# Kernel tuning notes

Measured on AMD Instinct MI355X. Metric: run time of the kernel, lower is better.

Reference implementation:

```python
import jax, jax.numpy as jnp
import numpy as np

T, B, NHID = 64, 32, 768
NB, BS = 6, 128          # num_blocks, block_size = nhid // num_blocks
TOPK = 4                 # active blocks per step
NTOK = 32000
ATT = 4 * BS             # input-attention value dim (att_out), per RIMs BlocksCore
DK = 64                  # input-attention key dim
NH2, DK2 = 4, 16         # communication attention heads / head dim


def setup_inputs() -> dict:
    key = jax.random.key(0)
    ks = jax.random.split(key, 16)
    s = 0.02
    return {
        "x": jax.random.normal(ks[0], (T, B, NHID), jnp.float32),
        "hx0": jax.random.normal(ks[1], (B, NHID), jnp.float32),
        "cx0": jax.random.normal(ks[2], (B, NHID), jnp.float32),
        # input attention (1 head): per-read-block query proj, per-write-slot key/value proj
        "Wq_in": jax.random.normal(ks[3], (NB, BS, DK), jnp.float32) * s,
        "Wk_in": jax.random.normal(ks[4], (2, NHID, DK), jnp.float32) * s,
        "Wv_in": jax.random.normal(ks[5], (2, NHID, ATT), jnp.float32) * s,
        # block-diagonal LSTM (blockify_params): per-block weights
        "Wih": jax.random.normal(ks[6], (NB, ATT, 4 * BS), jnp.float32) * s,
        "Whh": jax.random.normal(ks[7], (NB, BS, 4 * BS), jnp.float32) * s,
        "b_lstm": jnp.zeros((NB, 4 * BS), jnp.float32),
        # communication attention (4 heads, dk=dv=16), per-block projections + output proj
        "Wq_c": jax.random.normal(ks[8], (NB, BS, NH2 * DK2), jnp.float32) * s,
        "Wk_c": jax.random.normal(ks[9], (NB, BS, NH2 * DK2), jnp.float32) * s,
        "Wv_c": jax.random.normal(ks[10], (NB, BS, NH2 * DK2), jnp.float32) * s,
        "Wo_c": jax.random.normal(ks[11], (NB, NH2 * DK2, BS), jnp.float32) * s,
        # decoder
        "Wd": jax.random.normal(ks[12], (NTOK, NHID), jnp.float32) * 0.1,
        "bd": jnp.zeros((NTOK,), jnp.float32),
    }


def _step(hx, cx, xt, Wq_in, Wk_in, Wv_in, Wih, Whh, b_lstm, Wq_c, Wk_c, Wv_c, Wo_c):
    hb = hx.reshape(B, NB, BS)
    cb = cx.reshape(B, NB, BS)
    # --- input attention: each block reads from {null, input} slots ---
    kv_in = jnp.stack([jnp.zeros_like(xt), xt], axis=1)          # [B,2,NHID]
    q = jnp.einsum('bnd,ndk->bnk', hb, Wq_in)                    # [B,NB,DK]
    k = jnp.einsum('bmd,mdk->bmk', kv_in, Wk_in)                 # [B,2,DK]
    v = jnp.einsum('bmd,mdv->bmv', kv_in, Wv_in)                 # [B,2,ATT]
    iatt = jax.nn.softmax(
        jnp.einsum('bnk,bmk->bnm', q, k) / jnp.sqrt(jnp.float32(DK)), axis=-1)
    inp_use = jnp.einsum('bnm,bmv->bnv', iatt, v)                # [B,NB,ATT]
    # --- top-k block routing: drop NB-TOPK blocks attending most to null ---
    null_att = iatt[:, :, 0]                                     # [B,NB]
    _, drop_idx = jax.lax.top_k(null_att, NB - TOPK)
    mask = jnp.ones((B, NB), hx.dtype).at[
        jnp.arange(B)[:, None], drop_idx].set(0.0)               # [B,NB]
    # --- per-block (block-diagonal) LSTM ---
    gates = (jnp.einsum('bnv,nvg->bng', inp_use, Wih)
             + jnp.einsum('bnh,nhg->bng', hb, Whh) + b_lstm)     # [B,NB,4*BS]
    i, f, g, o = jnp.split(gates, 4, axis=-1)
    c_new = jax.nn.sigmoid(f) * cb + jax.nn.sigmoid(i) * jnp.tanh(g)
    h_new = jax.nn.sigmoid(o) * jnp.tanh(c_new)                  # [B,NB,BS]
    # --- communication attention among blocks (residual) ---
    q2 = jnp.einsum('bnd,ndk->bnk', h_new, Wq_c).reshape(B, NB, NH2, DK2)
    k2 = jnp.einsum('bnd,ndk->bnk', h_new, Wk_c).reshape(B, NB, NH2, DK2)
    v2 = jnp.einsum('bnd,ndk->bnk', h_new, Wv_c).reshape(B, NB, NH2, DK2)
    att = jax.nn.softmax(
        jnp.einsum('bihk,bjhk->bhij', q2, k2) / jnp.sqrt(jnp.float32(DK2)), axis=-1)
    comm = jnp.einsum('bhij,bjhv->bihv', att, v2).reshape(B, NB, NH2 * DK2)
    h_new = h_new + jnp.einsum('bnk,nkd->bnd', comm, Wo_c)
    # --- gated state update: inactive blocks keep old state ---
    m = mask[:, :, None]
    hx_next = (m * h_new + (1.0 - m) * hb).reshape(B, NHID)
    cx_next = (m * c_new + (1.0 - m) * cb).reshape(B, NHID)
    return hx_next, cx_next


def reference(x, hx0, cx0, Wq_in, Wk_in, Wv_in, Wih, Whh, b_lstm,
              Wq_c, Wk_c, Wv_c, Wo_c, Wd, bd):
    def scan_step(carry, xt):
        hx, cx = carry
        hx, cx = _step(hx, cx, xt, Wq_in, Wk_in, Wv_in, Wih, Whh, b_lstm,
                       Wq_c, Wk_c, Wv_c, Wo_c)
        return (hx, cx), hx
    (hx, cx), outs = jax.lax.scan(scan_step, (hx0, cx0), x)     # outs: [T,B,NHID]
    decoded = outs.reshape(T * B, NHID) @ Wd.T + bd              # [T*B,NTOK]
    return decoded, hx, cx
```

## Files before the change

kernel.cpp:

```cpp
#include <hip/hip_runtime.h>
#include <hip/hip_bf16.h>
#include <stdint.h>

#define TT 64
#define BB 32
#define NHIDC 768
#define NBK 6
#define BSZ 128
#define NTOKC 32000

using f32x4  = __attribute__((ext_vector_type(4))) float;
using f32x2  = __attribute__((ext_vector_type(2))) float;
using short8 = __attribute__((ext_vector_type(8))) short;
typedef unsigned long long u64;

#define OFF_XPUB  4096u
#define OFF_HTB   8065024u
#define OFF_K1    11210752u
#define OFF_V1    11735040u
#define OFF_U     15929344u
#define OFF_WDB   41095168u

__device__ __forceinline__ float sigf(float x){ return 1.f/(1.f + expf(-x)); }

__device__ __forceinline__ void stp(u64* p, float v, unsigned tag){
  union { float f; unsigned u; } cv; cv.f = v;
  const u64 pk = ((u64)tag << 32) | cv.u;
  __hip_atomic_store(p, pk, __ATOMIC_RELAXED, __HIP_MEMORY_SCOPE_AGENT);
}
__device__ __forceinline__ float ldp(const u64* p, unsigned tag){
  u64 v = __hip_atomic_load(p, __ATOMIC_RELAXED, __HIP_MEMORY_SCOPE_AGENT);
  while ((unsigned)(v >> 32) < tag){
    __builtin_amdgcn_s_sleep(1);
    v = __hip_atomic_load(p, __ATOMIC_RELAXED, __HIP_MEMORY_SCOPE_AGENT);
  }
  union { unsigned u; float f; } cv; cv.u = (unsigned)v;
  return cv.f;
}
#define CBAR asm volatile("" ::: "memory")

__device__ __forceinline__ void gload16(const void* g, void* l){
  __builtin_amdgcn_global_load_lds(
      (const __attribute__((address_space(1))) unsigned int*)g,
      (__attribute__((address_space(3))) unsigned int*)l, 16, 0, 0);
}

__device__ __forceinline__ int xslot(int par, int gg, int nn, int b){
  return (((par*16 + gg)*6 + nn)*2 + b)*132;
}

__global__ void prep_kernel(const float* __restrict__ Wd,
                            unsigned short* __restrict__ Wdb,
                            u64* __restrict__ xpub)
{
  {
    int i = blockIdx.x*blockDim.x + threadIdx.x;
    const int nx = 2*16*6*2*132;
    const int stride = gridDim.x*blockDim.x;
    for (; i < nx; i += stride)
      __hip_atomic_store(xpub + i, 0ull, __ATOMIC_RELAXED, __HIP_MEMORY_SCOPE_AGENT);
  }
  int i = blockIdx.x*blockDim.x + threadIdx.x;
  const int n4 = NTOKC*NHIDC/4;
  const int stride = gridDim.x*blockDim.x;
  for (; i < n4; i += stride){
    const float4 v = ((const float4*)Wd)[i];
    ushort4 o;
    __hip_bfloat16 b0 = __float2bfloat16(v.x); o.x = *reinterpret_cast<unsigned short*>(&b0);
    __hip_bfloat16 b1 = __float2bfloat16(v.y); o.y = *reinterpret_cast<unsigned short*>(&b1);
    __hip_bfloat16 b2 = __float2bfloat16(v.z); o.z = *reinterpret_cast<unsigned short*>(&b2);
    __hip_bfloat16 b3 = __float2bfloat16(v.w); o.w = *reinterpret_cast<unsigned short*>(&b3);
    ((ushort4*)Wdb)[i] = o;
  }
}

template<int TM, int TN>
__global__ __launch_bounds__(256) void gemm_f32(
    const float* __restrict__ A, int lda,
    const float* __restrict__ B, int ldb, long bstride,
    float* __restrict__ C, int ldc, long cstride,
    int N, int K)
{
  constexpr int BM = 16*TM, BN = 16*TN;
  __shared__ float As[16][BM];
  __shared__ float Bs[16][BN+4];
  const float* Bb = B + (long)blockIdx.z * bstride;
  float* Cb = C + (long)blockIdx.z * cstride;
  const int m0 = blockIdx.x*BM, n0 = blockIdx.y*BN;
  const int tid = threadIdx.x, tx = tid & 15, ty = tid >> 4;
  float acc[TM][TN];
  #pragma unroll
  for (int i=0;i<TM;++i)
    #pragma unroll
    for (int j=0;j<TN;++j) acc[i][j]=0.f;

  for (int k0=0; k0<K; k0+=16){
    if constexpr (TM == 8){
      const int r = tid>>1, kk = (tid&1)*8;
      const float4 v0 = *(const float4*)&A[(long)(m0+r)*lda + k0 + kk];
      const float4 v1 = *(const float4*)&A[(long)(m0+r)*lda + k0 + kk + 4];
      As[kk+0][r]=v0.x; As[kk+1][r]=v0.y; As[kk+2][r]=v0.z; As[kk+3][r]=v0.w;
      As[kk+4][r]=v1.x; As[kk+5][r]=v1.y; As[kk+6][r]=v1.z; As[kk+7][r]=v1.w;
    } else {
      const int r = tid>>2, kk = (tid&3)*4;
      const float4 v0 = *(const float4*)&A[(long)(m0+r)*lda + k0 + kk];
      As[kk+0][r]=v0.x; As[kk+1][r]=v0.y; As[kk+2][r]=v0.z; As[kk+3][r]=v0.w;
    }
    if constexpr (TN == 8){
      const int rb = tid>>4, cb = (tid&15)*8;
      float4 v0 = {0,0,0,0}, v1 = {0,0,0,0};
      if (n0+cb+4 <= N) v0 = *(const float4*)&Bb[(long)(k0+rb)*ldb + n0+cb];
      if (n0+cb+8 <= N) v1 = *(const float4*)&Bb[(long)(k0+rb)*ldb + n0+cb+4];
      *(float4*)&Bs[rb][cb]   = v0;
      *(float4*)&Bs[rb][cb+4] = v1;
    } else {
      const int rb = tid>>4, cb = (tid&15)*4;
      float4 v0 = {0,0,0,0};
      if (n0+cb+4 <= N) v0 = *(const float4*)&Bb[(long)(k0+rb)*ldb + n0+cb];
      *(float4*)&Bs[rb][cb] = v0;
    }
    __syncthreads();
    #pragma unroll
    for (int kk=0; kk<16; ++kk){
      float av[TM], bv[TN];
      #pragma unroll
      for (int i=0;i<TM;++i) av[i] = As[kk][ty*TM+i];
      #pragma unroll
      for (int j=0;j<TN;++j) bv[j] = Bs[kk][tx*TN+j];
      #pragma unroll
      for (int i=0;i<TM;++i)
        #pragma unroll
        for (int j=0;j<TN;++j) acc[i][j] += av[i]*bv[j];
    }
    __syncthreads();
  }
  #pragma unroll
  for (int i=0;i<TM;++i){
    const int row = m0 + ty*TM + i;
    #pragma unroll
    for (int j=0;j<TN;++j){
      const int col = n0 + tx*TN + j;
      if (col < N) Cb[(long)row*ldc + col] = acc[i][j];
    }
  }
}

__global__ __launch_bounds__(1024, 2) void recurrent_kernel(
    const float* __restrict__ hx0, const float* __restrict__ cx0,
    const float* __restrict__ Wq_in, const float* __restrict__ Whh,
    const float* __restrict__ b_lstm,
    const float* __restrict__ Wk_c, const float* __restrict__ Wv_c,
    const float* __restrict__ Wq_c, const float* __restrict__ Wo_c,
    const float* __restrict__ K1buf, const float* __restrict__ Ubuf,
    u64* __restrict__ xpub,
    unsigned short* __restrict__ HTx,
    float* __restrict__ out_hx, float* __restrict__ out_cx)
{
  const int w = blockIdx.x, gg = w/6, n = w - gg*6, tid = threadIdx.x;

  __shared__ float WcT[192*130];
  __shared__ float WqL[128*65];
  __shared__ float hL[2][128], cL[2][128], h0L[2][128], cnL[2][128];
  __shared__ float partL[2][2][512];
  __shared__ float uL[2][512];
  __shared__ float blL[512];
  __shared__ float kvqL[2][192];
  __shared__ float kvAll[2][6][130];
  __shared__ float commL[2][64];
  __shared__ float nullAll[2][8];
  __shared__ float sL[2], nullLoc[2], maskL[2];

  const int kh = tid >> 9, gc = tid & 511;
  const int od = tid >> 3, okq = tid & 7;

  f32x4 whr[16];
  {
    const float* src = Whh + (long)n*65536 + kh*64*512 + gc;
    #pragma unroll
    for (int r4=0; r4<16; ++r4){
      f32x4 v;
      v[0] = src[(r4*4+0)*512]; v[1] = src[(r4*4+1)*512];
      v[2] = src[(r4*4+2)*512]; v[3] = src[(r4*4+3)*512];
      whr[r4] = v;
    }
  }
  #pragma unroll
  for (int i=0;i<16;++i) asm volatile("" : "+v"(whr[i]));
  f32x4 wo0, wo1;
  {
    const float* src = Wo_c + n*8192 + od;
    #pragma unroll
    for (int j=0;j<4;++j) wo0[j] = src[(okq*8+j)*128];
    #pragma unroll
    for (int j=0;j<4;++j) wo1[j] = src[(okq*8+4+j)*128];
  }
  asm volatile("" : "+v"(wo0));
  asm volatile("" : "+v"(wo1));

  if (tid < 512) blL[tid] = b_lstm[n*512 + tid];
  for (int i = tid; i < 8192; i += 1024){
    const int h = i>>6, c = i&63;
    WcT[(c    )*130 + h] = Wk_c[n*8192 + i];
    WcT[(c+ 64)*130 + h] = Wv_c[n*8192 + i];
    WcT[(c+128)*130 + h] = Wq_c[n*8192 + i];
    WqL[h*65 + c] = Wq_in[n*8192 + i];
  }
  if (tid < 256){
    const int b = tid>>7, d = tid&127;
    hL[b][d] = hx0[(gg*2+b)*768 + n*128 + d];
    cL[b][d] = cx0[(gg*2+b)*768 + n*128 + d];
  }
  __syncthreads();

  for (int t = 0; t < TT; ++t){
    const int par = t & 1;
    const unsigned tag = (unsigned)(t+1);
    uL[kh][gc] = Ubuf[((long)(t*32 + gg*2 + kh)*6 + n)*512 + gc];
    float k1r = 0.f;
    if (tid < 128) k1r = K1buf[(long)(t*32 + gg*2 + (tid>>6))*64 + (tid&63)];

    {
      float gd0 = 0.f, gd1 = 0.f;
      #pragma unroll
      for (int r4 = 0; r4 < 16; ++r4){
        const f32x4 h0v = *(const f32x4*)&hL[0][kh*64 + r4*4];
        const f32x4 h1v = *(const f32x4*)&hL[1][kh*64 + r4*4];
        #pragma unroll
        for (int j=0;j<4;++j){
          gd0 += whr[r4][j]*h0v[j];
          gd1 += whr[r4][j]*h1v[j];
        }
      }
      partL[0][kh][gc] = gd0;
      partL[1][kh][gc] = gd1;
    }
    if (tid < 128){
      const int b = tid>>6, k = tid&63;
      float q = 0.f;
      #pragma unroll 16
      for (int h=0; h<128; ++h) q += WqL[h*65 + k]*hL[b][h];
      float term = q*k1r;
      #pragma unroll
      for (int off=32; off; off>>=1) term += __shfl_xor(term, off);
      if (k == 0){
        const float l1 = term*0.125f;
        const float mx = fmaxf(l1, 0.f);
        const float e0 = expf(0.f-mx), e1 = expf(l1-mx);
        const float inv = 1.f/(e0+e1);
        sL[b] = e1*inv;
        nullLoc[b] = e0*inv;
        stp(xpub + xslot(par,gg,n,b) + 128, e0*inv, tag);
      }
    }
    __syncthreads();
    if (tid < 256){
      const int b = tid>>7, dd = tid&127;
      const float s = sL[b];
      const float gi = partL[b][0][dd]     + partL[b][1][dd]     + s*uL[b][dd]     + blL[dd];
      const float gf = partL[b][0][128+dd] + partL[b][1][128+dd] + s*uL[b][128+dd] + blL[128+dd];
      const float gG = partL[b][0][256+dd] + partL[b][1][256+dd] + s*uL[b][256+dd] + blL[256+dd];
      const float go = partL[b][0][384+dd] + partL[b][1][384+dd] + s*uL[b][384+dd] + blL[384+dd];
      const float cp = cL[b][dd];
      const float cn = sigf(gf)*cp + sigf(gi)*tanhf(gG);
      const float h0 = sigf(go)*tanhf(cn);
      cnL[b][dd] = cn; h0L[b][dd] = h0;
    }
    __syncthreads();
    if (tid < 384){
      const int b = tid/192, c = tid%192;
      float a = 0.f;
      #pragma unroll
      for (int h4=0; h4<32; ++h4){
        const f32x2 wa = *(const f32x2*)&WcT[c*130 + h4*4];
        const f32x2 wb = *(const f32x2*)&WcT[c*130 + h4*4 + 2];
        const f32x4 hv = *(const f32x4*)&h0L[b][h4*4];
        a += wa[0]*hv[0] + wa[1]*hv[1] + wb[0]*hv[2] + wb[1]*hv[3];
      }
      kvqL[b][c] = a;
      if (c < 128) stp(xpub + xslot(par,gg,n,b) + c, a, tag);
    }
    __syncthreads();
    for (int idx = tid; idx < 1536; idx += 1024){
      const int j = idx/256, r = idx&255, b = r>>7, c = r&127;
      if (j == n) kvAll[b][j][c] = kvqL[b][c];
      else        kvAll[b][j][c] = ldp(xpub + xslot(par,gg,j,b) + c, tag);
    }
    if (tid < 12){
      const int j = tid>>1, b = tid&1;
      if (j == n) nullAll[b][j] = nullLoc[b];
      else        nullAll[b][j] = ldp(xpub + xslot(par,gg,j,b) + 128, tag);
    }
    __syncthreads(); CBAR;
    if (tid < 64){
      const int lane = tid;
      const int g5 = lane>>3, l3 = lane&7;
      const int b = g5>>2, h = g5&3;
      float lg = -1e30f;
      if (l3 < 6){
        float s = 0.f;
        #pragma unroll
        for (int kk=0; kk<16; ++kk)
          s += kvqL[b][128 + h*16 + kk]*kvAll[b][l3][h*16 + kk];
        lg = s*0.25f;
      }
      float mx = lg;
      mx = fmaxf(mx, __shfl_xor(mx,1));
      mx = fmaxf(mx, __shfl_xor(mx,2));
      mx = fmaxf(mx, __shfl_xor(mx,4));
      float ev = (l3 < 6) ? expf(lg - mx) : 0.f;
      float sum = ev;
      sum += __shfl_xor(sum,1); sum += __shfl_xor(sum,2); sum += __shfl_xor(sum,4);
      const float myw = ev/sum;
      float s0 = 0.f, s1 = 0.f;
      #pragma unroll
      for (int j=0;j<6;++j){
        const float wj = __shfl(myw, g5*8 + j);
        s0 += wj*kvAll[b][j][64 + h*16 + l3*2];
        s1 += wj*kvAll[b][j][64 + h*16 + l3*2 + 1];
      }
      commL[b][h*16 + l3*2]     = s0;
      commL[b][h*16 + l3*2 + 1] = s1;
      if (lane < 2){
        const float own = nullAll[lane][n];
        int rank = 0;
        #pragma unroll
        for (int j=0;j<6;++j){
          const float v = nullAll[lane][j];
          rank += (v > own || (v == own && j < n)) ? 1 : 0;
        }
        maskL[lane] = (rank < 2) ? 0.f : 1.f;
      }
    }
    __syncthreads();
    {
      #pragma unroll
      for (int b=0; b<2; ++b){
        float a = 0.f;
        #pragma unroll
        for (int j=0;j<4;++j) a += commL[b][okq*8+j]*wo0[j];
        #pragma unroll
        for (int j=0;j<4;++j) a += commL[b][okq*8+4+j]*wo1[j];
        a += __shfl_xor(a,1); a += __shfl_xor(a,2); a += __shfl_xor(a,4);
        if (okq == 0 && maskL[b] != 0.f){
          hL[b][od] = h0L[b][od] + a;
          cL[b][od] = cnL[b][od];
        }
      }
    }
    __syncthreads();
    if (tid < 256){
      const int b = tid>>7, d = tid&127;
      const float hv = hL[b][d];
      __hip_bfloat16 hb16 = __float2bfloat16(hv);
      HTx[(long)(t*32 + gg*2 + b)*768 + n*128 + d] = *reinterpret_cast<unsigned short*>(&hb16);
      if (t == TT-1){
        out_hx[(gg*2+b)*768 + n*128 + d] = hv;
        out_cx[(gg*2+b)*768 + n*128 + d] = cL[b][d];
      }
    }
  }
}

__global__ __launch_bounds__(256) void decoder_kernel(
    const unsigned short* __restrict__ A,
    const unsigned short* __restrict__ Bw,
    const float* __restrict__ bd,
    float* __restrict__ out)
{
  __shared__ unsigned short As[4096];
  __shared__ unsigned short Bs[4096];
  const int bid = blockIdx.x;
  const int tile = (bid & 7)*500 + (bid >> 3);
  const int m0 = (tile & 15)*128, n0 = (tile >> 4)*128;
  const int tid = threadIdx.x;
  const int wv = tid >> 6, lane = tid & 63;
  const int wm = wv >> 1, wn = wv & 1;
  const int r16 = lane & 15, krow = lane >> 4;

  f32x4 acc[4][4] = {};

  for (int k0 = 0; k0 < 768; k0 += 32){
    #pragma unroll
    for (int i=0; i<2; ++i){
      const int idx = i*256 + tid;
      const int row = idx >> 2, k8 = (idx & 3)*8;
      gload16(&A [(long)(m0+row)*768 + k0 + k8], (char*)As + i*4096 + wv*1024);
      gload16(&Bw[(long)(n0+row)*768 + k0 + k8], (char*)Bs + i*4096 + wv*1024);
    }
    __syncthreads();
    short8 af[4], bf[4];
    #pragma unroll
    for (int mi=0; mi<4; ++mi)
      af[mi] = *(const short8*)&As[(wm*64 + mi*16 + r16)*32 + krow*8];
    #pragma unroll
    for (int ni=0; ni<4; ++ni)
      bf[ni] = *(const short8*)&Bs[(wn*64 + ni*16 + r16)*32 + krow*8];
    #pragma unroll
    for (int mi=0; mi<4; ++mi)
      #pragma unroll
      for (int ni=0; ni<4; ++ni)
        acc[mi][ni] = __builtin_amdgcn_mfma_f32_16x16x32_bf16(af[mi], bf[ni], acc[mi][ni], 0, 0, 0);
    __syncthreads();
  }

  #pragma unroll
  for (int ni=0; ni<4; ++ni){
    const int col = n0 + wn*64 + ni*16 + r16;
    const float bv = bd[col];
    #pragma unroll
    for (int mi=0; mi<4; ++mi){
      const int rbase = m0 + wm*64 + mi*16 + krow*4;
      #pragma unroll
      for (int j=0; j<4; ++j)
        out[(size_t)(rbase + j)*NTOKC + col] = acc[mi][ni][j] + bv;
    }
  }
}

extern "C" void kernel_launch(void* const* d_in, const int* in_sizes, int n_in,
                              void* d_out, int out_size, void* d_ws, size_t ws_size,
                              hipStream_t stream)
{
  (void)in_sizes; (void)n_in; (void)out_size; (void)ws_size;
  const float* x      = (const float*)d_in[0];
  const float* hx0    = (const float*)d_in[1];
  const float* cx0    = (const float*)d_in[2];
  const float* Wq_in  = (const float*)d_in[3];
  const float* Wk_in  = (const float*)d_in[4];
  const float* Wv_in  = (const float*)d_in[5];
  const float* Wih    = (const float*)d_in[6];
  const float* Whh    = (const float*)d_in[7];
  const float* b_lstm = (const float*)d_in[8];
  const float* Wq_c   = (const float*)d_in[9];
  const float* Wk_c   = (const float*)d_in[10];
  const float* Wv_c   = (const float*)d_in[11];
  const float* Wo_c   = (const float*)d_in[12];
  const float* Wd     = (const float*)d_in[13];
  const float* bd     = (const float*)d_in[14];

  char* ws = (char*)d_ws;
  u64*           xpub = (u64*)(ws + OFF_XPUB);
  unsigned short* HTx = (unsigned short*)(ws + OFF_HTB);
  float*         K1b  = (float*)(ws + OFF_K1);
  float*         V1b  = (float*)(ws + OFF_V1);
  float*         Ub   = (float*)(ws + OFF_U);
  unsigned short* Wdb = (unsigned short*)(ws + OFF_WDB);

  float* out_dec = (float*)d_out;
  float* out_hx  = out_dec + (size_t)2048*NTOKC;
  float* out_cx  = out_hx + BB*NHIDC;

  prep_kernel<<<2048, 256, 0, stream>>>(Wd, Wdb, xpub);
  gemm_f32<4,4><<<dim3(32,1,1), 256, 0, stream>>>(x, NHIDC, Wk_in + 768*64, 64, 0,
                                                  K1b, 64, 0, 64, NHIDC);
  gemm_f32<4,4><<<dim3(32,8,1), 256, 0, stream>>>(x, NHIDC, Wv_in + 768*512, 512, 0,
                                                  V1b, 512, 0, 512, NHIDC);
  gemm_f32<8,8><<<dim3(16,4,6), 256, 0, stream>>>(V1b, 512, Wih, 512, (long)512*512,
                                                  Ub, 3072, 512, 512, 512);
  recurrent_kernel<<<96, 1024, 0, stream>>>(hx0, cx0, Wq_in, Whh, b_lstm,
                                            Wk_c, Wv_c, Wq_c, Wo_c,
                                            K1b, Ub, xpub, HTx,
                                            out_hx, out_cx);
  decoder_kernel<<<4000, 256, 0, stream>>>(HTx, Wdb, bd, out_dec);
}
```

Measured before the change: 1.273 ms.

## Fuse all stages into a persistent mega-kernel overlapping recurrence with decoder

Replaces the separate prep, projection GEMMs, recurrent and decoder launches with one persistent kernel. 96 blocks run the recurrence while 160 worker blocks convert Wd to bf16, compute the input projections, and then pull decoder tiles dynamically. Each decoder tile waits on per-4-step counters, so the decoder for finished timesteps overlaps the remaining recurrence. The intent is to hide the decoder and prep work behind the serial recurrence and remove launch gaps. The cost is spin-wait synchronisation through global atomics and a co-residency assumption for all 256 blocks, which can deadlock if they are not all resident.

```diff
diff --git a/kernel.cpp b/kernel.cpp
--- a/kernel.cpp
+++ b/kernel.cpp
@@ -8,12 +8,16 @@
 #define NBK 6
 #define BSZ 128
 #define NTOKC 32000
+#define NREC 96
+#define NWRK 160
+#define NWG  256
 
 using f32x4  = __attribute__((ext_vector_type(4))) float;
 using f32x2  = __attribute__((ext_vector_type(2))) float;
 using short8 = __attribute__((ext_vector_type(8))) short;
 typedef unsigned long long u64;
 
+#define OFF_CTR   0u
 #define OFF_XPUB  4096u
 #define OFF_HTB   8065024u
 #define OFF_K1    11210752u
@@ -37,6 +41,13 @@
   union { unsigned u; float f; } cv; cv.u = (unsigned)v;
   return cv.f;
 }
+__device__ __forceinline__ void stc(float* p, float v){
+  __hip_atomic_store(p, v, __ATOMIC_RELAXED, __HIP_MEMORY_SCOPE_AGENT);
+}
+__device__ __forceinline__ void waitc(unsigned int* p, unsigned tgt){
+  while (__hip_atomic_load(p, __ATOMIC_RELAXED, __HIP_MEMORY_SCOPE_AGENT) < tgt)
+    __builtin_amdgcn_s_sleep(2);
+}
 #define CBAR asm volatile("" ::: "memory")
 
 __device__ __forceinline__ void gload16(const void* g, void* l){
@@ -49,45 +60,50 @@
   return (((par*16 + gg)*6 + nn)*2 + b)*132;
 }
 
-__global__ void prep_kernel(const float* __restrict__ Wd,
-                            unsigned short* __restrict__ Wdb,
-                            u64* __restrict__ xpub)
-{
-  {
-    int i = blockIdx.x*blockDim.x + threadIdx.x;
-    const int nx = 2*16*6*2*132;
-    const int stride = gridDim.x*blockDim.x;
-    for (; i < nx; i += stride)
-      __hip_atomic_store(xpub + i, 0ull, __ATOMIC_RELAXED, __HIP_MEMORY_SCOPE_AGENT);
-  }
+struct RecS {
+  float WcT[192*130];
+  float WqL[128*65];
+  float hL[2][128], cL[2][128], h0L[2][128], cnL[2][128];
+  float partL[2][2][512];
+  float uL[2][512];
+  float blL[512];
+  float kvqL[2][192];
+  float kvAll[2][6][130];
+  float commL[2][64];
+  float nullAll[2][8];
+  float sL[2], nullLoc[2], maskL[2];
+};
+struct WrkS {
+  union {
+    struct { float As[4][16][128]; float Bs[4][16][132]; } g8;
+    struct { float As[4][16][64];  float Bs[4][16][68];  } g4;
+    struct { unsigned short As[4][4096]; unsigned short Bs[4][4096]; } d;
+  };
+  int bcast;
+};
+union SmemU { RecS r; WrkS w; };
+
+__global__ void prep0_kernel(unsigned int* __restrict__ ctr, u64* __restrict__ xpub){
   int i = blockIdx.x*blockDim.x + threadIdx.x;
-  const int n4 = NTOKC*NHIDC/4;
+  if (i < 64)
+    __hip_atomic_store(&ctr[i], 0u, __ATOMIC_RELAXED, __HIP_MEMORY_SCOPE_AGENT);
+  const int nx = 2*16*6*2*132;
   const int stride = gridDim.x*blockDim.x;
-  for (; i < n4; i += stride){
-    const float4 v = ((const float4*)Wd)[i];
-    ushort4 o;
-    __hip_bfloat16 b0 = __float2bfloat16(v.x); o.x = *reinterpret_cast<unsigned short*>(&b0);
-    __hip_bfloat16 b1 = __float2bfloat16(v.y); o.y = *reinterpret_cast<unsigned short*>(&b1);
-    __hip_bfloat16 b2 = __float2bfloat16(v.z); o.z = *reinterpret_cast<unsigned short*>(&b2);
-    __hip_bfloat16 b3 = __float2bfloat16(v.w); o.w = *reinterpret_cast<unsigned short*>(&b3);
-    ((ushort4*)Wdb)[i] = o;
-  }
+  for (int j = i; j < nx; j += stride)
+    __hip_atomic_store(&xpub[j], 0ull, __ATOMIC_RELAXED, __HIP_MEMORY_SCOPE_AGENT);
 }
 
 template<int TM, int TN>
-__global__ __launch_bounds__(256) void gemm_f32(
-    const float* __restrict__ A, int lda,
-    const float* __restrict__ B, int ldb, long bstride,
-    float* __restrict__ C, int ldc, long cstride,
-    int N, int K)
+__device__ void gemm_unit(const float* __restrict__ A, int lda,
+                          const float* __restrict__ Bb, int ldb,
+                          float* __restrict__ Cb, int ldc,
+                          int N, int K, int m0, int n0, bool active,
+                          float* AsP, float* BsP, int ltid)
 {
   constexpr int BM = 16*TM, BN = 16*TN;
-  __shared__ float As[16][BM];
-  __shared__ float Bs[16][BN+4];
-  const float* Bb = B + (long)blockIdx.z * bstride;
-  float* Cb = C + (long)blockIdx.z * cstride;
-  const int m0 = blockIdx.x*BM, n0 = blockIdx.y*BN;
-  const int tid = threadIdx.x, tx = tid & 15, ty = tid >> 4;
+  float (*As)[BM]   = reinterpret_cast<float(*)[BM]>(AsP);
+  float (*Bs)[BN+4] = reinterpret_cast<float(*)[BN+4]>(BsP);
+  const int tx = ltid & 15, ty = ltid >> 4;
   float acc[TM][TN];
   #pragma unroll
   for (int i=0;i<TM;++i)
@@ -96,25 +112,25 @@
 
   for (int k0=0; k0<K; k0+=16){
     if constexpr (TM == 8){
-      const int r = tid>>1, kk = (tid&1)*8;
+      const int r = ltid>>1, kk = (ltid&1)*8;
       const float4 v0 = *(const float4*)&A[(long)(m0+r)*lda + k0 + kk];
       const float4 v1 = *(const float4*)&A[(long)(m0+r)*lda + k0 + kk + 4];
       As[kk+0][r]=v0.x; As[kk+1][r]=v0.y; As[kk+2][r]=v0.z; As[kk+3][r]=v0.w;
       As[kk+4][r]=v1.x; As[kk+5][r]=v1.y; As[kk+6][r]=v1.z; As[kk+7][r]=v1.w;
     } else {
-      const int r = tid>>2, kk = (tid&3)*4;
+      const int r = ltid>>2, kk = (ltid&3)*4;
       const float4 v0 = *(const float4*)&A[(long)(m0+r)*lda + k0 + kk];
       As[kk+0][r]=v0.x; As[kk+1][r]=v0.y; As[kk+2][r]=v0.z; As[kk+3][r]=v0.w;
     }
     if constexpr (TN == 8){
-      const int rb = tid>>4, cb = (tid&15)*8;
+      const int rb = ltid>>4, cb = (ltid&15)*8;
       float4 v0 = {0,0,0,0}, v1 = {0,0,0,0};
       if (n0+cb+4 <= N) v0 = *(const float4*)&Bb[(long)(k0+rb)*ldb + n0+cb];
       if (n0+cb+8 <= N) v1 = *(const float4*)&Bb[(long)(k0+rb)*ldb + n0+cb+4];
       *(float4*)&Bs[rb][cb]   = v0;
       *(float4*)&Bs[rb][cb+4] = v1;
     } else {
-      const int rb = tid>>4, cb = (tid&15)*4;
+      const int rb = ltid>>4, cb = (ltid&15)*4;
       float4 v0 = {0,0,0,0};
       if (n0+cb+4 <= N) v0 = *(const float4*)&Bb[(long)(k0+rb)*ldb + n0+cb];
       *(float4*)&Bs[rb][cb] = v0;
@@ -134,267 +150,47 @@
     }
     __syncthreads();
   }
-  #pragma unroll
-  for (int i=0;i<TM;++i){
-    const int row = m0 + ty*TM + i;
-    #pragma unroll
-    for (int j=0;j<TN;++j){
-      const int col = n0 + tx*TN + j;
-      if (col < N) Cb[(long)row*ldc + col] = acc[i][j];
+  if (active){
+    #pragma unroll
+    for (int i=0;i<TM;++i){
+      const int row = m0 + ty*TM + i;
+      #pragma unroll
+      for (int j=0;j<TN;++j){
+        const int col = n0 + tx*TN + j;
+        if (col < N) stc(&Cb[(long)row*ldc + col], acc[i][j]);
+      }
     }
   }
 }
 
-__global__ __launch_bounds__(1024, 2) void recurrent_kernel(
-    const float* __restrict__ hx0, const float* __restrict__ cx0,
-    const float* __restrict__ Wq_in, const float* __restrict__ Whh,
-    const float* __restrict__ b_lstm,
-    const float* __restrict__ Wk_c, const float* __restrict__ Wv_c,
-    const float* __restrict__ Wq_c, const float* __restrict__ Wo_c,
-    const float* __restrict__ K1buf, const float* __restrict__ Ubuf,
-    u64* __restrict__ xpub,
-    unsigned short* __restrict__ HTx,
-    float* __restrict__ out_hx, float* __restrict__ out_cx)
+__device__ void decoder_unit(const unsigned short* __restrict__ A,
+                             const unsigned short* __restrict__ Bw,
+                             const float* __restrict__ bd,
+                             float* __restrict__ out,
+                             int m0, int n0,
+                             unsigned short* AsP, unsigned short* BsP, int ltid)
 {
-  const int w = blockIdx.x, gg = w/6, n = w - gg*6, tid = threadIdx.x;
-
-  __shared__ float WcT[192*130];
-  __shared__ float WqL[128*65];
-  __shared__ float hL[2][128], cL[2][128], h0L[2][128], cnL[2][128];
-  __shared__ float partL[2][2][512];
-  __shared__ float uL[2][512];
-  __shared__ float blL[512];
-  __shared__ float kvqL[2][192];
-  __shared__ float kvAll[2][6][130];
-  __shared__ float commL[2][64];
-  __shared__ float nullAll[2][8];
-  __shared__ float sL[2], nullLoc[2], maskL[2];
-
-  const int kh = tid >> 9, gc = tid & 511;
-  const int od = tid >> 3, okq = tid & 7;
-
-  f32x4 whr[16];
-  {
-    const float* src = Whh + (long)n*65536 + kh*64*512 + gc;
-    #pragma unroll
-    for (int r4=0; r4<16; ++r4){
-      f32x4 v;
-      v[0] = src[(r4*4+0)*512]; v[1] = src[(r4*4+1)*512];
-      v[2] = src[(r4*4+2)*512]; v[3] = src[(r4*4+3)*512];
-      whr[r4] = v;
-    }
-  }
-  #pragma unroll
-  for (int i=0;i<16;++i) asm volatile("" : "+v"(whr[i]));
-  f32x4 wo0, wo1;
-  {
-    const float* src = Wo_c + n*8192 + od;
-    #pragma unroll
-    for (int j=0;j<4;++j) wo0[j] = src[(okq*8+j)*128];
-    #pragma unroll
-    for (int j=0;j<4;++j) wo1[j] = src[(okq*8+4+j)*128];
-  }
-  asm volatile("" : "+v"(wo0));
-  asm volatile("" : "+v"(wo1));
-
-  if (tid < 512) blL[tid] = b_lstm[n*512 + tid];
-  for (int i = tid; i < 8192; i += 1024){
-    const int h = i>>6, c = i&63;
-    WcT[(c    )*130 + h] = Wk_c[n*8192 + i];
-    WcT[(c+ 64)*130 + h] = Wv_c[n*8192 + i];
-    WcT[(c+128)*130 + h] = Wq_c[n*8192 + i];
-    WqL[h*65 + c] = Wq_in[n*8192 + i];
-  }
-  if (tid < 256){
-    const int b = tid>>7, d = tid&127;
-    hL[b][d] = hx0[(gg*2+b)*768 + n*128 + d];
-    cL[b][d] = cx0[(gg*2+b)*768 + n*128 + d];
-  }
-  __syncthreads();
-
-  for (int t = 0; t < TT; ++t){
-    const int par = t & 1;
-    const unsigned tag = (unsigned)(t+1);
-    uL[kh][gc] = Ubuf[((long)(t*32 + gg*2 + kh)*6 + n)*512 + gc];
-    float k1r = 0.f;
-    if (tid < 128) k1r = K1buf[(long)(t*32 + gg*2 + (tid>>6))*64 + (tid&63)];
-
-    {
-      float gd0 = 0.f, gd1 = 0.f;
-      #pragma unroll
-      for (int r4 = 0; r4 < 16; ++r4){
-        const f32x4 h0v = *(const f32x4*)&hL[0][kh*64 + r4*4];
-        const f32x4 h1v = *(const f32x4*)&hL[1][kh*64 + r4*4];
-        #pragma unroll
-        for (int j=0;j<4;++j){
-          gd0 += whr[r4][j]*h0v[j];
-          gd1 += whr[r4][j]*h1v[j];
-        }
-      }
-      partL[0][kh][gc] = gd0;
-      partL[1][kh][gc] = gd1;
-    }
-    if (tid < 128){
-      const int b = tid>>6, k = tid&63;
-      float q = 0.f;
-      #pragma unroll 16
-      for (int h=0; h<128; ++h) q += WqL[h*65 + k]*hL[b][h];
-      float term = q*k1r;
-      #pragma unroll
-      for (int off=32; off; off>>=1) term += __shfl_xor(term, off);
-      if (k == 0){
-        const float l1 = term*0.125f;
-        const float mx = fmaxf(l1, 0.f);
-        const float e0 = expf(0.f-mx), e1 = expf(l1-mx);
-        const float inv = 1.f/(e0+e1);
-        sL[b] = e1*inv;
-        nullLoc[b] = e0*inv;
-        stp(xpub + xslot(par,gg,n,b) + 128, e0*inv, tag);
-      }
-    }
-    __syncthreads();
-    if (tid < 256){
-      const int b = tid>>7, dd = tid&127;
-      const float s = sL[b];
-      const float gi = partL[b][0][dd]     + partL[b][1][dd]     + s*uL[b][dd]     + blL[dd];
-      const float gf = partL[b][0][128+dd] + partL[b][1][128+dd] + s*uL[b][128+dd] + blL[128+dd];
-      const float gG = partL[b][0][256+dd] + partL[b][1][256+dd] + s*uL[b][256+dd] + blL[256+dd];
-      const float go = partL[b][0][384+dd] + partL[b][1][384+dd] + s*uL[b][384+dd] + blL[384+dd];
-      const float cp = cL[b][dd];
-      const float cn = sigf(gf)*cp + sigf(gi)*tanhf(gG);
-      const float h0 = sigf(go)*tanhf(cn);
-      cnL[b][dd] = cn; h0L[b][dd] = h0;
-    }
-    __syncthreads();
-    if (tid < 384){
-      const int b = tid/192, c = tid%192;
-      float a = 0.f;
-      #pragma unroll
-      for (int h4=0; h4<32; ++h4){
-        const f32x2 wa = *(const f32x2*)&WcT[c*130 + h4*4];
-        const f32x2 wb = *(const f32x2*)&WcT[c*130 + h4*4 + 2];
-        const f32x4 hv = *(const f32x4*)&h0L[b][h4*4];
-        a += wa[0]*hv[0] + wa[1]*hv[1] + wb[0]*hv[2] + wb[1]*hv[3];
-      }
-      kvqL[b][c] = a;
-      if (c < 128) stp(xpub + xslot(par,gg,n,b) + c, a, tag);
-    }
-    __syncthreads();
-    for (int idx = tid; idx < 1536; idx += 1024){
-      const int j = idx/256, r = idx&255, b = r>>7, c = r&127;
-      if (j == n) kvAll[b][j][c] = kvqL[b][c];
-      else        kvAll[b][j][c] = ldp(xpub + xslot(par,gg,j,b) + c, tag);
-    }
-    if (tid < 12){
-      const int j = tid>>1, b = tid&1;
-      if (j == n) nullAll[b][j] = nullLoc[b];
-      else        nullAll[b][j] = ldp(xpub + xslot(par,gg,j,b) + 128, tag);
-    }
-    __syncthreads(); CBAR;
-    if (tid < 64){
-      const int lane = tid;
-      const int g5 = lane>>3, l3 = lane&7;
-      const int b = g5>>2, h = g5&3;
-      float lg = -1e30f;
-      if (l3 < 6){
-        float s = 0.f;
-        #pragma unroll
-        for (int kk=0; kk<16; ++kk)
-          s += kvqL[b][128 + h*16 + kk]*kvAll[b][l3][h*16 + kk];
-        lg = s*0.25f;
-      }
-      float mx = lg;
-      mx = fmaxf(mx, __shfl_xor(mx,1));
-      mx = fmaxf(mx, __shfl_xor(mx,2));
-      mx = fmaxf(mx, __shfl_xor(mx,4));
-      float ev = (l3 < 6) ? expf(lg - mx) : 0.f;
-      float sum = ev;
-      sum += __shfl_xor(sum,1); sum += __shfl_xor(sum,2); sum += __shfl_xor(sum,4);
-      const float myw = ev/sum;
-      float s0 = 0.f, s1 = 0.f;
-      #pragma unroll
-      for (int j=0;j<6;++j){
-        const float wj = __shfl(myw, g5*8 + j);
-        s0 += wj*kvAll[b][j][64 + h*16 + l3*2];
-        s1 += wj*kvAll[b][j][64 + h*16 + l3*2 + 1];
-      }
-      commL[b][h*16 + l3*2]     = s0;
-      commL[b][h*16 + l3*2 + 1] = s1;
-      if (lane < 2){
-        const float own = nullAll[lane][n];
-        int rank = 0;
-        #pragma unroll
-        for (int j=0;j<6;++j){
-          const float v = nullAll[lane][j];
-          rank += (v > own || (v == own && j < n)) ? 1 : 0;
-        }
-        maskL[lane] = (rank < 2) ? 0.f : 1.f;
-      }
-    }
-    __syncthreads();
-    {
-      #pragma unroll
-      for (int b=0; b<2; ++b){
-        float a = 0.f;
-        #pragma unroll
-        for (int j=0;j<4;++j) a += commL[b][okq*8+j]*wo0[j];
-        #pragma unroll
-        for (int j=0;j<4;++j) a += commL[b][okq*8+4+j]*wo1[j];
-        a += __shfl_xor(a,1); a += __shfl_xor(a,2); a += __shfl_xor(a,4);
-        if (okq == 0 && maskL[b] != 0.f){
-          hL[b][od] = h0L[b][od] + a;
-          cL[b][od] = cnL[b][od];
-        }
-      }
-    }
-    __syncthreads();
-    if (tid < 256){
-      const int b = tid>>7, d = tid&127;
-      const float hv = hL[b][d];
-      __hip_bfloat16 hb16 = __float2bfloat16(hv);
-      HTx[(long)(t*32 + gg*2 + b)*768 + n*128 + d] = *reinterpret_cast<unsigned short*>(&hb16);
-      if (t == TT-1){
-        out_hx[(gg*2+b)*768 + n*128 + d] = hv;
-        out_cx[(gg*2+b)*768 + n*128 + d] = cL[b][d];
-      }
-    }
-  }
-}
-
-__global__ __launch_bounds__(256) void decoder_kernel(
-    const unsigned short* __restrict__ A,
-    const unsigned short* __restrict__ Bw,
-    const float* __restrict__ bd,
-    float* __restrict__ out)
-{
-  __shared__ unsigned short As[4096];
-  __shared__ unsigned short Bs[4096];
-  const int bid = blockIdx.x;
-  const int tile = (bid & 7)*500 + (bid >> 3);
-  const int m0 = (tile & 15)*128, n0 = (tile >> 4)*128;
-  const int tid = threadIdx.x;
-  const int wv = tid >> 6, lane = tid & 63;
+  const int wv = ltid >> 6, lane = ltid & 63;
   const int wm = wv >> 1, wn = wv & 1;
   const int r16 = lane & 15, krow = lane >> 4;
-
   f32x4 acc[4][4] = {};
 
   for (int k0 = 0; k0 < 768; k0 += 32){
     #pragma unroll
     for (int i=0; i<2; ++i){
-      const int idx = i*256 + tid;
+      const int idx = i*256 + ltid;
       const int row = idx >> 2, k8 = (idx & 3)*8;
-      gload16(&A [(long)(m0+row)*768 + k0 + k8], (char*)As + i*4096 + wv*1024);
-      gload16(&Bw[(long)(n0+row)*768 + k0 + k8], (char*)Bs + i*4096 + wv*1024);
+      gload16(&A [(long)(m0+row)*768 + k0 + k8], (char*)AsP + i*4096 + wv*1024);
+      gload16(&Bw[(long)(n0+row)*768 + k0 + k8], (char*)BsP + i*4096 + wv*1024);
     }
     __syncthreads();
     short8 af[4], bf[4];
     #pragma unroll
     for (int mi=0; mi<4; ++mi)
-      af[mi] = *(const short8*)&As[(wm*64 + mi*16 + r16)*32 + krow*8];
+      af[mi] = *(const short8*)&AsP[(wm*64 + mi*16 + r16)*32 + krow*8];
     #pragma unroll
     for (int ni=0; ni<4; ++ni)
-      bf[ni] = *(const short8*)&Bs[(wn*64 + ni*16 + r16)*32 + krow*8];
+      bf[ni] = *(const short8*)&BsP[(wn*64 + ni*16 + r16)*32 + krow*8];
     #pragma unroll
     for (int mi=0; mi<4; ++mi)
       #pragma unroll
@@ -413,6 +209,296 @@
       #pragma unroll
       for (int j=0; j<4; ++j)
         out[(size_t)(rbase + j)*NTOKC + col] = acc[mi][ni][j] + bv;
+    }
+  }
+}
+
+__global__ __launch_bounds__(1024, 2) void mega_kernel(
+    const float* __restrict__ x,
+    const float* __restrict__ hx0, const float* __restrict__ cx0,
+    const float* __restrict__ Wq_in, const float* __restrict__ Wk_in,
+    const float* __restrict__ Wv_in, const float* __restrict__ Wih,
+    const float* __restrict__ Whh, const float* __restrict__ b_lstm,
+    const float* __restrict__ Wk_c, const float* __restrict__ Wv_c,
+    const float* __restrict__ Wq_c, const float* __restrict__ Wo_c,
+    const float* __restrict__ Wd, const float* __restrict__ bd,
+    unsigned int* __restrict__ ctr, u64* __restrict__ xpub,
+    float* __restrict__ K1buf, float* __restrict__ V1buf, float* __restrict__ Ubuf,
+    unsigned short* __restrict__ Wdb, unsigned short* __restrict__ HTx,
+    float* __restrict__ out_dec, float* __restrict__ out_hx, float* __restrict__ out_cx)
+{
+  __shared__ SmemU smem;
+  const int bid = blockIdx.x, tid = threadIdx.x;
+
+  if (bid < NREC){
+    RecS& Z = smem.r;
+    const int gg = bid & 15, n = bid >> 4;
+    const int kh = tid >> 9, gc = tid & 511;
+    const int od = tid >> 3, okq = tid & 7;
+
+    f32x4 whr[16];
+    {
+      const float* src = Whh + (long)n*65536 + kh*64*512 + gc;
+      #pragma unroll
+      for (int r4=0; r4<16; ++r4){
+        f32x4 v;
+        v[0] = src[(r4*4+0)*512]; v[1] = src[(r4*4+1)*512];
+        v[2] = src[(r4*4+2)*512]; v[3] = src[(r4*4+3)*512];
+        whr[r4] = v;
+      }
+    }
+    #pragma unroll
+    for (int i=0;i<16;++i) asm volatile("" : "+v"(whr[i]));
+    f32x4 wo0, wo1;
+    {
+      const float* src = Wo_c + n*8192 + od;
+      #pragma unroll
+      for (int j=0;j<4;++j) wo0[j] = src[(okq*8+j)*128];
+      #pragma unroll
+      for (int j=0;j<4;++j) wo1[j] = src[(okq*8+4+j)*128];
+    }
+    asm volatile("" : "+v"(wo0));
+    asm volatile("" : "+v"(wo1));
+
+    if (tid < 512) Z.blL[tid] = b_lstm[n*512 + tid];
+    for (int i = tid; i < 8192; i += 1024){
+      const int h = i>>6, c = i&63;
+      Z.WcT[(c    )*130 + h] = Wk_c[n*8192 + i];
+      Z.WcT[(c+ 64)*130 + h] = Wv_c[n*8192 + i];
+      Z.WcT[(c+128)*130 + h] = Wq_c[n*8192 + i];
+      Z.WqL[h*65 + c] = Wq_in[n*8192 + i];
+    }
+    if (tid < 256){
+      const int b = tid>>7, d = tid&127;
+      Z.hL[b][d] = hx0[(gg*2+b)*768 + n*128 + d];
+      Z.cL[b][d] = cx0[(gg*2+b)*768 + n*128 + d];
+    }
+    __syncthreads();
+
+    for (int t = 0; t < TT; ++t){
+      const int par = t & 1;
+      const unsigned tag = (unsigned)(t+1);
+
+      if ((t & 3) == 0){
+        if (tid == 0) waitc(&ctr[2 + (t>>2)], 24u);
+        __syncthreads(); CBAR;
+      }
+      Z.uL[kh][gc] = Ubuf[((long)(t*32 + gg*2 + kh)*6 + n)*512 + gc];
+      float k1r = 0.f;
+      if (tid < 128) k1r = K1buf[(long)(t*32 + gg*2 + (tid>>6))*64 + (tid&63)];
+
+      {
+        float gd0 = 0.f, gd1 = 0.f;
+        #pragma unroll
+        for (int r4 = 0; r4 < 16; ++r4){
+          const f32x4 h0v = *(const f32x4*)&Z.hL[0][kh*64 + r4*4];
+          const f32x4 h1v = *(const f32x4*)&Z.hL[1][kh*64 + r4*4];
+          #pragma unroll
+          for (int j=0;j<4;++j){
+            gd0 += whr[r4][j]*h0v[j];
+            gd1 += whr[r4][j]*h1v[j];
+          }
+        }
+        Z.partL[0][kh][gc] = gd0;
+        Z.partL[1][kh][gc] = gd1;
+      }
+      if (tid < 128){
+        const int b = tid>>6, k = tid&63;
+        float q = 0.f;
+        #pragma unroll 16
+        for (int h=0; h<128; ++h) q += Z.WqL[h*65 + k]*Z.hL[b][h];
+        float term = q*k1r;
+        #pragma unroll
+        for (int off=32; off; off>>=1) term += __shfl_xor(term, off);
+        if (k == 0){
+          const float l1 = term*0.125f;
+          const float mx = fmaxf(l1, 0.f);
+          const float e0 = expf(0.f-mx), e1 = expf(l1-mx);
+          const float inv = 1.f/(e0+e1);
+          Z.sL[b] = e1*inv;
+          Z.nullLoc[b] = e0*inv;
+          stp(xpub + xslot(par,gg,n,b) + 128, e0*inv, tag);
+        }
+      }
+      __syncthreads();
+      if (tid < 256){
+        const int b = tid>>7, dd = tid&127;
+        const float s = Z.sL[b];
+        const float gi = Z.partL[b][0][dd]     + Z.partL[b][1][dd]     + s*Z.uL[b][dd]     + Z.blL[dd];
+        const float gf = Z.partL[b][0][128+dd] + Z.partL[b][1][128+dd] + s*Z.uL[b][128+dd] + Z.blL[128+dd];
+        const float gG = Z.partL[b][0][256+dd] + Z.partL[b][1][256+dd] + s*Z.uL[b][256+dd] + Z.blL[256+dd];
+        const float go = Z.partL[b][0][384+dd] + Z.partL[b][1][384+dd] + s*Z.uL[b][384+dd] + Z.blL[384+dd];
+        const float cp = Z.cL[b][dd];
+        const float cn = sigf(gf)*cp + sigf(gi)*tanhf(gG);
+        const float h0 = sigf(go)*tanhf(cn);
+        Z.cnL[b][dd] = cn; Z.h0L[b][dd] = h0;
+      }
+      __syncthreads();
+      if (tid < 384){
+        const int b = tid/192, c = tid%192;
+        float a = 0.f;
+        #pragma unroll
+        for (int h4=0; h4<32; ++h4){
+          const f32x2 wa = *(const f32x2*)&Z.WcT[c*130 + h4*4];
+          const f32x2 wb = *(const f32x2*)&Z.WcT[c*130 + h4*4 + 2];
+          const f32x4 hv = *(const f32x4*)&Z.h0L[b][h4*4];
+          a += wa[0]*hv[0] + wa[1]*hv[1] + wb[0]*hv[2] + wb[1]*hv[3];
+        }
+        Z.kvqL[b][c] = a;
+        if (c < 128) stp(xpub + xslot(par,gg,n,b) + c, a, tag);
+      }
+      __syncthreads();
+      for (int idx = tid; idx < 1536; idx += 1024){
+        const int j = idx/256, r = idx&255, b = r>>7, c = r&127;
+        if (j == n) Z.kvAll[b][j][c] = Z.kvqL[b][c];
+        else        Z.kvAll[b][j][c] = ldp(xpub + xslot(par,gg,j,b) + c, tag);
+      }
+      if (tid < 12){
+        const int j = tid>>1, b = tid&1;
+        if (j == n) Z.nullAll[b][j] = Z.nullLoc[b];
+        else        Z.nullAll[b][j] = ldp(xpub + xslot(par,gg,j,b) + 128, tag);
+      }
+      __syncthreads(); CBAR;
+      if (tid < 64){
+        const int lane = tid;
+        const int g5 = lane>>3, l3 = lane&7;
+        const int b = g5>>2, h = g5&3;
+        float lg = -1e30f;
+        if (l3 < 6){
+          float s = 0.f;
+          #pragma unroll
+          for (int kk=0; kk<16; ++kk)
+            s += Z.kvqL[b][128 + h*16 + kk]*Z.kvAll[b][l3][h*16 + kk];
+          lg = s*0.25f;
+        }
+        float mx = lg;
+        mx = fmaxf(mx, __shfl_xor(mx,1));
+        mx = fmaxf(mx, __shfl_xor(mx,2));
+        mx = fmaxf(mx, __shfl_xor(mx,4));
+        float ev = (l3 < 6) ? expf(lg - mx) : 0.f;
+        float sum = ev;
+        sum += __shfl_xor(sum,1); sum += __shfl_xor(sum,2); sum += __shfl_xor(sum,4);
+        const float myw = ev/sum;
+        float s0 = 0.f, s1 = 0.f;
+        #pragma unroll
+        for (int j=0;j<6;++j){
+          const float wj = __shfl(myw, g5*8 + j);
+          s0 += wj*Z.kvAll[b][j][64 + h*16 + l3*2];
+          s1 += wj*Z.kvAll[b][j][64 + h*16 + l3*2 + 1];
+        }
+        Z.commL[b][h*16 + l3*2]     = s0;
+        Z.commL[b][h*16 + l3*2 + 1] = s1;
+        if (lane < 2){
+          const float own = Z.nullAll[lane][n];
+          int rank = 0;
+          #pragma unroll
+          for (int j=0;j<6;++j){
+            const float v = Z.nullAll[lane][j];
+            rank += (v > own || (v == own && j < n)) ? 1 : 0;
+          }
+          Z.maskL[lane] = (rank < 2) ? 0.f : 1.f;
+        }
+      }
+      __syncthreads();
+      {
+        #pragma unroll
+        for (int b=0; b<2; ++b){
+          float a = 0.f;
+          #pragma unroll
+          for (int j=0;j<4;++j) a += Z.commL[b][okq*8+j]*wo0[j];
+          #pragma unroll
+          for (int j=0;j<4;++j) a += Z.commL[b][okq*8+4+j]*wo1[j];
+          a += __shfl_xor(a,1); a += __shfl_xor(a,2); a += __shfl_xor(a,4);
+          if (okq == 0 && Z.maskL[b] != 0.f){
+            Z.hL[b][od] = Z.h0L[b][od] + a;
+            Z.cL[b][od] = Z.cnL[b][od];
+          }
+        }
+      }
+      __syncthreads();
+      if (tid < 128){
+        const int b = tid >> 6, q = tid & 63;
+        const float v0 = Z.hL[b][2*q], v1 = Z.hL[b][2*q+1];
+        __hip_bfloat16 x0 = __float2bfloat16(v0), x1 = __float2bfloat16(v1);
+        unsigned pk = (unsigned)*reinterpret_cast<unsigned short*>(&x0)
+                    | ((unsigned)*reinterpret_cast<unsigned short*>(&x1) << 16);
+        __hip_atomic_store((unsigned int*)HTx + ((long)(t*32 + gg*2 + b)*384 + n*64 + q),
+                           pk, __ATOMIC_RELAXED, __HIP_MEMORY_SCOPE_AGENT);
+      }
+      if (t == TT-1 && tid < 256){
+        const int b = tid>>7, d = tid&127;
+        out_hx[(gg*2+b)*768 + n*128 + d] = Z.hL[b][d];
+        out_cx[(gg*2+b)*768 + n*128 + d] = Z.cL[b][d];
+      }
+      if ((t & 3) == 3){
+        __syncthreads();
+        if (tid == 0)
+          __hip_atomic_fetch_add(&ctr[18 + (t>>2)], 1u, __ATOMIC_RELAXED, __HIP_MEMORY_SCOPE_AGENT);
+      }
+    }
+  } else {
+    WrkS& W = smem.w;
+    const int wid = bid - NREC;
+    const int sub = tid >> 8, ltid = tid & 255;
+
+    {
+      const long n4 = (long)NTOKC*NHIDC/4;
+      for (long i = (long)wid*1024 + tid; i < n4; i += (long)NWRK*1024){
+        const float4 v = ((const float4*)Wd)[i];
+        __hip_bfloat16 b0=__float2bfloat16(v.x), b1=__float2bfloat16(v.y),
+                       b2=__float2bfloat16(v.z), b3=__float2bfloat16(v.w);
+        u64 pk = (u64)*reinterpret_cast<unsigned short*>(&b0)
+               | ((u64)*reinterpret_cast<unsigned short*>(&b1) << 16)
+               | ((u64)*reinterpret_cast<unsigned short*>(&b2) << 32)
+               | ((u64)*reinterpret_cast<unsigned short*>(&b3) << 48);
+        __hip_atomic_store((u64*)Wdb + i, pk, __ATOMIC_RELAXED, __HIP_MEMORY_SCOPE_AGENT);
+      }
+    }
+    if (wid*4 < 288){
+      const int u = wid*4 + sub;
+      const bool act = u < 288;
+      const int uc = act ? u : wid*4;
+      const float* Bu; float* Cu; int ldb, ldc, N, m0, n0;
+      if (uc < 32){ Bu = Wk_in + 768*64; Cu = K1buf; ldb = 64;  ldc = 64;  N = 64;
+                    m0 = uc*64; n0 = 0; }
+      else        { const int v = uc - 32;
+                    Bu = Wv_in + 768*512; Cu = V1buf; ldb = 512; ldc = 512; N = 512;
+                    m0 = (v>>3)*64; n0 = (v&7)*64; }
+      gemm_unit<4,4>(x, 768, Bu, ldb, Cu, ldc, N, 768, m0, n0, act,
+                     &W.g4.As[sub][0][0], &W.g4.Bs[sub][0][0], ltid);
+    }
+    __syncthreads();
+    if (tid == 0)
+      __hip_atomic_fetch_add(&ctr[0], 1u, __ATOMIC_RELAXED, __HIP_MEMORY_SCOPE_AGENT);
+    if (tid == 0) waitc(&ctr[0], (unsigned)NWRK);
+    __syncthreads(); CBAR;
+
+    if (wid < 96){
+      const int u = wid*4 + sub;
+      const int m = u/24, r = u%24, nt = r/6, z = r%6;
+      gemm_unit<8,8>(V1buf, 512, Wih + (long)z*262144, 512,
+                     Ubuf + (long)z*512, 3072, 512, 512, m*128, nt*128, true,
+                     &W.g8.As[sub][0][0], &W.g8.Bs[sub][0][0], ltid);
+      __syncthreads();
+      if (tid == 0)
+        __hip_atomic_fetch_add(&ctr[2 + (wid*4)/24], 4u, __ATOMIC_RELAXED, __HIP_MEMORY_SCOPE_AGENT);
+    }
+    __syncthreads();
+
+    for (;;){
+      if (tid == 0)
+        W.bcast = (int)__hip_atomic_fetch_add(&ctr[1], 4u, __ATOMIC_RELAXED, __HIP_MEMORY_SCOPE_AGENT);
+      __syncthreads();
+      const int t0 = W.bcast;
+      if (t0 >= 4000) break;
+      const int mneed = (t0 + 3) / 250;
+      if (tid == 0) waitc(&ctr[18 + mneed], (unsigned)NREC);
+      __syncthreads(); CBAR;
+      const int ts = t0 + sub;
+      const int m0 = (ts/250)*128, n0 = (ts%250)*128;
+      decoder_unit(HTx, Wdb, bd, out_dec, m0, n0,
+                   &W.d.As[sub][0], &W.d.Bs[sub][0], ltid);
+      __syncthreads();
     }
   }
 }
@@ -439,6 +525,7 @@
   const float* bd     = (const float*)d_in[14];
 
   char* ws = (char*)d_ws;
+  unsigned int*  ctr  = (unsigned int*)(ws + OFF_CTR);
   u64*           xpub = (u64*)(ws + OFF_XPUB);
   unsigned short* HTx = (unsigned short*)(ws + OFF_HTB);
   float*         K1b  = (float*)(ws + OFF_K1);
@@ -450,16 +537,9 @@
   float* out_hx  = out_dec + (size_t)2048*NTOKC;
   float* out_cx  = out_hx + BB*NHIDC;
 
-  prep_kernel<<<2048, 256, 0, stream>>>(Wd, Wdb, xpub);
-  gemm_f32<4,4><<<dim3(32,1,1), 256, 0, stream>>>(x, NHIDC, Wk_in + 768*64, 64, 0,
-                                                  K1b, 64, 0, 64, NHIDC);
-  gemm_f32<4,4><<<dim3(32,8,1), 256, 0, stream>>>(x, NHIDC, Wv_in + 768*512, 512, 0,
-                                                  V1b, 512, 0, 512, NHIDC);
-  gemm_f32<8,8><<<dim3(16,4,6), 256, 0, stream>>>(V1b, 512, Wih, 512, (long)512*512,
-                                                  Ub, 3072, 512, 512, 512);
-  recurrent_kernel<<<96, 1024, 0, stream>>>(hx0, cx0, Wq_in, Whh, b_lstm,
-                                            Wk_c, Wv_c, Wq_c, Wo_c,
-                                            K1b, Ub, xpub, HTx,
-                                            out_hx, out_cx);
-  decoder_kernel<<<4000, 256, 0, stream>>>(HTx, Wdb, bd, out_dec);
-}
+  prep0_kernel<<<64, 256, 0, stream>>>(ctr, xpub);
+  mega_kernel<<<NWG, 1024, 0, stream>>>(x, hx0, cx0, Wq_in, Wk_in, Wv_in, Wih,
+                                        Whh, b_lstm, Wk_c, Wv_c, Wq_c, Wo_c,
+                                        Wd, bd, ctr, xpub, K1b, V1b, Ub,
+                                        Wdb, HTx, out_dec, out_hx, out_cx);
+}
```

Result: slower. 2.030 ms (+59.4%).
